# Kernel tuning notes

Hardware: AMD Instinct MI355X
Metric: run time of the kernel (lower is better)

The kernel has to match this reference:

```python
import jax, jax.numpy as jnp
import numpy as np
import math

E, DK, R = 8, 32, 16        # n_experts, d_k, lora rank
SCALING = 16.0 / 16.0        # lora_alpha / r


def setup_inputs() -> dict:
    key = jax.random.key(0)
    ks = jax.random.split(key, 7)
    Bt, S, Din, Dout = 4, 2048, 4096, 4096
    x = jax.random.normal(ks[0], (Bt, S, Din), jnp.float32)
    W = jax.random.normal(ks[1], (Dout, Din), jnp.float32) * 0.02   # base linear weight
    b = jnp.zeros((Dout,), jnp.float32)
    Wq = jax.random.normal(ks[2], (E * DK, Din), jnp.float32) * 0.02  # query_layer
    Wk = jax.random.normal(ks[3], (E * DK, Din), jnp.float32) * 0.02  # key_layer
    A = jax.random.normal(ks[4], (E, R, Din), jnp.float32) * 0.02     # lora_As stacked
    Bm = jax.random.normal(ks[5], (E, Dout, R), jnp.float32) * 0.02   # lora_Bs stacked (nonzero for testing)
    return {"x": x, "W": W, "b": b, "Wq": Wq, "Wk": Wk, "A": A, "Bm": Bm}


def reference(x, W, b, Wq, Wk, A, Bm):
    Bt, S, Din = x.shape
    # base linear: y = x @ W.T + b
    result = jnp.einsum('bsi,oi->bso', x, W) + b
    # per-expert attention routing scores
    q = jnp.einsum('bsi,ni->bsn', x, Wq).reshape(Bt, S, E, DK)
    k = jnp.einsum('bsi,ni->bsn', x, Wk).reshape(Bt, S, E, DK)
    scores = jnp.einsum('bsed,bsed->bse', q, k) / math.sqrt(DK)
    w = jax.nn.softmax(scores, axis=-1)                      # [b,s,E]
    # per-expert low-rank projection: [b,s,E,r]
    h = jnp.einsum('bsi,eri->bser', x, A)
    # fused weighted combine through lora_B: avoids [b,s,E,out] intermediate
    combined = jnp.einsum('bse,bser,eor->bso', w, h, Bm) * SCALING
    return result + combined
```

## Files before the change

### kernel.cpp

```cpp
#include <hip/hip_runtime.h>
#include <hip/hip_bf16.h>
#include <cstdint>
#include <cstddef>


#define T_TOK   8192
#define DIN     4096
#define DOUT    4096
#define KEXT    4224
#define NQKA    640
#define SCALING 1.0f

typedef __attribute__((ext_vector_type(8))) short bf16x8;
typedef __attribute__((ext_vector_type(4))) float f32x4;

__device__ __forceinline__ unsigned short f2bf(float f) {
    __hip_bfloat16 h = __float2bfloat16(f);
    return *reinterpret_cast<unsigned short*>(&h);
}

__device__ __forceinline__ void load_lds16(const void* g, void* l) {
    __builtin_amdgcn_global_load_lds((__attribute__((address_space(1))) void*)g,
                                     (__attribute__((address_space(3))) void*)l,
                                     16, 0, 0);
}

__global__ __launch_bounds__(256) void conv_x(const float4* __restrict__ x,
                                              unsigned short* __restrict__ Aext) {
    int t = blockIdx.x * 256 + threadIdx.x;
    int row = t >> 10, c4 = t & 1023;
    float4 v = x[(size_t)row * 1024 + c4];
    ushort4 o;
    o.x = f2bf(v.x); o.y = f2bf(v.y); o.z = f2bf(v.z); o.w = f2bf(v.w);
    *(ushort4*)&Aext[(size_t)row * KEXT + c4 * 4] = o;
}

__global__ __launch_bounds__(256) void conv_w(const float4* __restrict__ W,
                                              unsigned short* __restrict__ Wext) {
    int t = blockIdx.x * 256 + threadIdx.x;
    int row = t >> 10, c4 = t & 1023;
    float4 v = W[(size_t)row * 1024 + c4];
    ushort4 o;
    o.x = f2bf(v.x); o.y = f2bf(v.y); o.z = f2bf(v.z); o.w = f2bf(v.w);
    *(ushort4*)&Wext[(size_t)row * KEXT + c4 * 4] = o;
}

__global__ __launch_bounds__(256) void fill_bm(const float* __restrict__ Bm,
                                               unsigned short* __restrict__ Wext) {
    int t = blockIdx.x * 256 + threadIdx.x;
    int o = t >> 7, j = t & 127;
    int e = j >> 4, r = j & 15;
    float v = Bm[(size_t)e * (DOUT * 16) + (size_t)o * 16 + r] * SCALING;
    Wext[(size_t)o * KEXT + DIN + j] = f2bf(v);
}

__global__ __launch_bounds__(256) void conv_wqka(const float4* __restrict__ Wq,
                                                 const float4* __restrict__ Wk,
                                                 const float4* __restrict__ Alora,
                                                 unsigned short* __restrict__ Wqka) {
    int t = blockIdx.x * 256 + threadIdx.x;
    int row = t >> 10, c4 = t & 1023;
    float4 v;
    if (row < 256)       v = Wq[(size_t)row * 1024 + c4];
    else if (row < 512)  v = Wk[(size_t)(row - 256) * 1024 + c4];
    else                 v = Alora[(size_t)(row - 512) * 1024 + c4];
    ushort4 o;
    o.x = f2bf(v.x); o.y = f2bf(v.y); o.z = f2bf(v.z); o.w = f2bf(v.w);
    *(ushort4*)&Wqka[(size_t)row * 4096 + c4 * 4] = o;
}

__global__ __launch_bounds__(64) void routing(const float* __restrict__ P,
                                              unsigned short* __restrict__ Aext) {
    int token = blockIdx.x;
    const float* p = P + (size_t)token * NQKA;
    int l = threadIdx.x;
    int e = l >> 3, s = l & 7;
    float pp = 0.f;
#pragma unroll
    for (int j = 0; j < 4; j++) {
        int d = e * 32 + s * 4 + j;
        pp += p[d] * p[256 + d];
    }
    pp += __shfl_xor(pp, 4);
    pp += __shfl_xor(pp, 2);
    pp += __shfl_xor(pp, 1);
    float score = pp * 0.17677669529663687f;
    float mx = score;
    mx = fmaxf(mx, __shfl_xor(mx, 8));
    mx = fmaxf(mx, __shfl_xor(mx, 16));
    mx = fmaxf(mx, __shfl_xor(mx, 32));
    float ex = expf(score - mx);
    float sm = ex;
    sm += __shfl_xor(sm, 8);
    sm += __shfl_xor(sm, 16);
    sm += __shfl_xor(sm, 32);
    float w = ex / sm;
    __shared__ float sw[8];
    if (s == 0) sw[e] = w;
    __syncthreads();
    unsigned short* g = Aext + (size_t)token * KEXT + DIN;
#pragma unroll
    for (int i = 0; i < 2; i++) {
        int j = l + i * 64;
        float val = sw[j >> 4] * p[512 + j] * SCALING;
        g[j] = f2bf(val);
    }
}

__global__ __launch_bounds__(256, 2)
void gemm_bt(const unsigned short* __restrict__ A,
             const unsigned short* __restrict__ B,
             float* __restrict__ C,
             const float* __restrict__ bias,
             int lda, int ldb, int N, int K) {
    __shared__ unsigned short ldsA[128 * 32];
    __shared__ unsigned short ldsB[128 * 32];
    const int t = threadIdx.x;
    const int m0 = blockIdx.y * 128;
    const int n0 = blockIdx.x * 128;
    const int wave = t >> 6, lane = t & 63;
    const int wm = (wave >> 1) * 64, wn = (wave & 1) * 64;
    const int fr = lane & 15, quad = lane >> 4;

    f32x4 acc[4][4];
#pragma unroll
    for (int i = 0; i < 4; i++)
#pragma unroll
        for (int j = 0; j < 4; j++) acc[i][j] = (f32x4){0.f, 0.f, 0.f, 0.f};

    const unsigned short* aptr = A + (size_t)(m0 + (t >> 2)) * lda + (t & 3) * 8;
    const unsigned short* bptr = B + (size_t)(n0 + (t >> 2)) * ldb + (t & 3) * 8;
    char* ldsAb = (char*)ldsA + t * 16;
    char* ldsBb = (char*)ldsB + t * 16;

    for (int k0 = 0; k0 < K; k0 += 32) {
        load_lds16(aptr, ldsAb);
        load_lds16(aptr + 64 * (size_t)lda, ldsAb + 4096);
        load_lds16(bptr, ldsBb);
        load_lds16(bptr + 64 * (size_t)ldb, ldsBb + 4096);
        aptr += 32; bptr += 32;
        __syncthreads();

        bf16x8 af[4], bfr[4];
#pragma unroll
        for (int i = 0; i < 4; i++)
            af[i] = *(const bf16x8*)(ldsA + (wm + i * 16 + fr) * 32 + quad * 8);
#pragma unroll
        for (int j = 0; j < 4; j++)
            bfr[j] = *(const bf16x8*)(ldsB + (wn + j * 16 + fr) * 32 + quad * 8);
#pragma unroll
        for (int i = 0; i < 4; i++)
#pragma unroll
            for (int j = 0; j < 4; j++)
                acc[i][j] = __builtin_amdgcn_mfma_f32_16x16x32_bf16(af[i], bfr[j], acc[i][j], 0, 0, 0);
        __syncthreads();
    }

#pragma unroll
    for (int j = 0; j < 4; j++) {
        int col = n0 + wn + j * 16 + fr;
        float bv = bias ? bias[col] : 0.f;
#pragma unroll
        for (int i = 0; i < 4; i++) {
            int row0 = m0 + wm + i * 16 + quad * 4;
#pragma unroll
            for (int r = 0; r < 4; r++)
                C[(size_t)(row0 + r) * N + col] = acc[i][j][r] + bv;
        }
    }
}

__global__ __launch_bounds__(512, 2)
void gemm256_8p(const unsigned short* __restrict__ A,
                const unsigned short* __restrict__ B,
                float* __restrict__ C,
                const float* __restrict__ bias,
                int lda, int ldb, int N, int K, int grid_n) {
    __shared__ unsigned short lds[65536];
    const int t = threadIdx.x;

    const int nwg = gridDim.x;
    const int q8 = nwg >> 3;
    const int wg = (blockIdx.x & 7) * q8 + (blockIdx.x >> 3);
    const int m0 = (wg / grid_n) * 256;
    const int n0 = (wg % grid_n) * 256;

    const int lane = t & 63;
    const int fr = lane & 15, quad = lane >> 4;
    const int wr = t >> 8;
    const int wc = (t >> 6) & 3;
    const int slot16 = ((quad ^ ((fr >> 1) & 3)) << 4);

    char* ldsA = (char*)lds;
    char* ldsB = (char*)lds + 65536;

    const int srow = t >> 2;
    const int sE = ((t & 3) ^ ((t >> 3) & 3)) * 8;
    const unsigned short* aP = A + (size_t)(m0 + srow) * lda + sE;
    const unsigned short* bP = B + (size_t)(n0 + srow) * ldb + sE;
    const size_t a128 = 128 * (size_t)lda, b128 = 128 * (size_t)ldb;
    char* dA = ldsA + t * 16;
    char* dB = ldsB + t * 16;

#define STAGE_A(cc) { const unsigned short* g_ = aP + (size_t)(cc) * 32;          \
        char* d_ = dA + ((cc) & 3) * 16384;                                       \
        load_lds16(g_, d_); load_lds16(g_ + a128, d_ + 8192); }
#define STAGE_B(cc) { const unsigned short* g_ = bP + (size_t)(cc) * 32;          \
        char* d_ = dB + ((cc) & 3) * 16384;                                       \
        load_lds16(g_, d_); load_lds16(g_ + b128, d_ + 8192); }

    f32x4 acc[8][4];
#pragma unroll
    for (int i = 0; i < 8; i++)
#pragma unroll
        for (int j = 0; j < 4; j++) acc[i][j] = (f32x4){0.f, 0.f, 0.f, 0.f};

    STAGE_A(0); STAGE_B(0);
    STAGE_A(1); STAGE_B(1);
    STAGE_A(2); STAGE_B(2);
    asm volatile("s_waitcnt vmcnt(8)" ::: "memory");
    __builtin_amdgcn_s_barrier();

    const int NC = K >> 5;
    const char* rA = ldsA + wr * 8192 + fr * 64 + slot16;
    const char* rB = ldsB + wc * 4096 + fr * 64 + slot16;

    for (int c = 0; c < NC; ++c) {
        const char* cA = rA + (c & 3) * 16384;
        const char* cB = rB + (c & 3) * 16384;
        bf16x8 am[4], bn[4];

#pragma unroll
        for (int i = 0; i < 4; ++i) am[i] = *(const bf16x8*)(cA + i * 1024);
#pragma unroll
        for (int i = 0; i < 4; ++i) bn[i] = *(const bf16x8*)(cB + i * 1024);
        if (c + 3 < NC) STAGE_A(c + 3);
        __builtin_amdgcn_sched_barrier(0);
        __builtin_amdgcn_s_barrier();
        asm volatile("s_waitcnt lgkmcnt(0)" ::: "memory");
        __builtin_amdgcn_sched_barrier(0);
        __builtin_amdgcn_s_setprio(1);
#pragma unroll
        for (int mf = 0; mf < 4; ++mf)
#pragma unroll
            for (int nf = 0; nf < 4; ++nf)
                acc[mf][nf] = __builtin_amdgcn_mfma_f32_16x16x32_bf16(am[mf], bn[nf], acc[mf][nf], 0, 0, 0);
        __builtin_amdgcn_s_setprio(0);
        __builtin_amdgcn_sched_barrier(0);
        __builtin_amdgcn_s_barrier();

#pragma unroll
        for (int i = 0; i < 4; ++i) am[i] = *(const bf16x8*)(cA + (4 + i) * 1024);
        if (c + 3 < NC) STAGE_B(c + 3);
        __builtin_amdgcn_sched_barrier(0);
        __builtin_amdgcn_s_barrier();
        asm volatile("s_waitcnt lgkmcnt(0)" ::: "memory");
        __builtin_amdgcn_sched_barrier(0);
        __builtin_amdgcn_s_setprio(1);
#pragma unroll
        for (int mf = 0; mf < 4; ++mf)
#pragma unroll
            for (int nf = 0; nf < 4; ++nf)
                acc[4 + mf][nf] = __builtin_amdgcn_mfma_f32_16x16x32_bf16(am[mf], bn[nf], acc[4 + mf][nf], 0, 0, 0);
        __builtin_amdgcn_s_setprio(0);
        if (c < NC - 3)       { asm volatile("s_waitcnt vmcnt(8)" ::: "memory"); }
        else if (c == NC - 3) { asm volatile("s_waitcnt vmcnt(4)" ::: "memory"); }
        else if (c == NC - 2) { asm volatile("s_waitcnt vmcnt(0)" ::: "memory"); }
        __builtin_amdgcn_sched_barrier(0);
        __builtin_amdgcn_s_barrier();
    }

#pragma unroll
    for (int nf = 0; nf < 4; ++nf) {
        int col = n0 + wc * 64 + nf * 16 + fr;
        float bv = bias ? bias[col] : 0.f;
#pragma unroll
        for (int mf = 0; mf < 8; ++mf) {
            int row0 = m0 + wr * 128 + mf * 16 + quad * 4;
#pragma unroll
            for (int r = 0; r < 4; ++r)
                C[(size_t)(row0 + r) * N + col] = acc[mf][nf][r] + bv;
        }
    }
#undef STAGE_A
#undef STAGE_B
}

extern "C" void kernel_launch(void* const* d_in, const int* in_sizes, int n_in,
                              void* d_out, int out_size, void* d_ws, size_t ws_size,
                              hipStream_t stream) {
    const float* x  = (const float*)d_in[0];
    const float* W  = (const float*)d_in[1];
    const float* b  = (const float*)d_in[2];
    const float* Wq = (const float*)d_in[3];
    const float* Wk = (const float*)d_in[4];
    const float* Al = (const float*)d_in[5];
    const float* Bm = (const float*)d_in[6];
    float* out = (float*)d_out;

    char* ws = (char*)d_ws;
    unsigned short* Aext = (unsigned short*)ws;
    unsigned short* Wext = (unsigned short*)(ws + 69206016);
    unsigned short* Wqka = (unsigned short*)(ws + 69206016 + 34603008);
    float*          P    = (float*)(ws + 69206016 + 34603008 + 5242880);

    conv_x   <<<T_TOK * 1024 / 256, 256, 0, stream>>>((const float4*)x, Aext);
    conv_w   <<<DOUT * 1024 / 256, 256, 0, stream>>>((const float4*)W, Wext);
    fill_bm  <<<DOUT * 128 / 256, 256, 0, stream>>>(Bm, Wext);
    conv_wqka<<<NQKA * 1024 / 256, 256, 0, stream>>>((const float4*)Wq, (const float4*)Wk,
                                                     (const float4*)Al, Wqka);

    {
        dim3 grid(NQKA / 128, T_TOK / 128);
        gemm_bt<<<grid, 256, 0, stream>>>(Aext, Wqka, P, nullptr, KEXT, 4096, NQKA, 4096);
    }

    routing<<<T_TOK, 64, 0, stream>>>(P, Aext);

    {
        int grid_n = DOUT / 256;
        int nwg = (T_TOK / 256) * grid_n;
        gemm256_8p<<<nwg, 512, 0, stream>>>(Aext, Wext, out, b, KEXT, KEXT, DOUT, KEXT, grid_n);
    }
}
```

Baseline: 640.5 us.

## Switch main GEMM to 32x32x16 MFMA with single-phase K loop

The main 256x256 GEMM replaces 16x16x32 bf16 MFMAs with 32x32x16 MFMAs, so each wave holds 4x2 32x32 accumulator tiles instead of 8x4 16x16 tiles. The two half-step phases per K chunk, each with its own barriers, are merged into one phase that reads all A and B fragments and issues both global-to-LDS stages together. This cuts LDS fragment reads and barrier count per chunk. It raises the number of live fragment registers and changes the LDS swizzle read pattern, which could cause bank conflicts or register pressure.

```diff
diff --git a/kernel.cpp b/kernel.cpp
--- a/kernel.cpp
+++ b/kernel.cpp
@@ -13,6 +13,7 @@
 
 typedef __attribute__((ext_vector_type(8))) short bf16x8;
 typedef __attribute__((ext_vector_type(4))) float f32x4;
+typedef __attribute__((ext_vector_type(16))) float f32x16;
 
 __device__ __forceinline__ unsigned short f2bf(float f) {
     __hip_bfloat16 h = __float2bfloat16(f);
@@ -171,7 +172,7 @@
 }
 
 __global__ __launch_bounds__(512, 2)
-void gemm256_8p(const unsigned short* __restrict__ A,
+void gemm256_32(const unsigned short* __restrict__ A,
                 const unsigned short* __restrict__ B,
                 float* __restrict__ C,
                 const float* __restrict__ bias,
@@ -186,10 +187,12 @@
     const int n0 = (wg % grid_n) * 256;
 
     const int lane = t & 63;
-    const int fr = lane & 15, quad = lane >> 4;
+    const int lrow = lane & 31, h = lane >> 5;
     const int wr = t >> 8;
     const int wc = (t >> 6) & 3;
-    const int slot16 = ((quad ^ ((fr >> 1) & 3)) << 4);
+    const int sw = (lrow >> 1) & 3;
+    const int off0 = (h ^ sw) << 4;
+    const int off1 = off0 ^ 32;
 
     char* ldsA = (char*)lds;
     char* ldsB = (char*)lds + 65536;
@@ -209,11 +212,13 @@
         char* d_ = dB + ((cc) & 3) * 16384;                                       \
         load_lds16(g_, d_); load_lds16(g_ + b128, d_ + 8192); }
 
-    f32x4 acc[8][4];
-#pragma unroll
-    for (int i = 0; i < 8; i++)
-#pragma unroll
-        for (int j = 0; j < 4; j++) acc[i][j] = (f32x4){0.f, 0.f, 0.f, 0.f};
+    f32x16 acc[4][2];
+#pragma unroll
+    for (int i = 0; i < 4; i++)
+#pragma unroll
+        for (int j = 0; j < 2; j++)
+#pragma unroll
+            for (int r = 0; r < 16; r++) acc[i][j][r] = 0.f;
 
     STAGE_A(0); STAGE_B(0);
     STAGE_A(1); STAGE_B(1);
@@ -222,46 +227,36 @@
     __builtin_amdgcn_s_barrier();
 
     const int NC = K >> 5;
-    const char* rA = ldsA + wr * 8192 + fr * 64 + slot16;
-    const char* rB = ldsB + wc * 4096 + fr * 64 + slot16;
+    const char* rA = ldsA + wr * 8192 + lrow * 64;
+    const char* rB = ldsB + wc * 4096 + lrow * 64;
 
     for (int c = 0; c < NC; ++c) {
         const char* cA = rA + (c & 3) * 16384;
         const char* cB = rB + (c & 3) * 16384;
-        bf16x8 am[4], bn[4];
-
-#pragma unroll
-        for (int i = 0; i < 4; ++i) am[i] = *(const bf16x8*)(cA + i * 1024);
-#pragma unroll
-        for (int i = 0; i < 4; ++i) bn[i] = *(const bf16x8*)(cB + i * 1024);
-        if (c + 3 < NC) STAGE_A(c + 3);
+        bf16x8 av[4][2], bv[2][2];
+#pragma unroll
+        for (int mt = 0; mt < 4; ++mt) {
+            av[mt][0] = *(const bf16x8*)(cA + mt * 2048 + off0);
+            av[mt][1] = *(const bf16x8*)(cA + mt * 2048 + off1);
+        }
+#pragma unroll
+        for (int nt = 0; nt < 2; ++nt) {
+            bv[nt][0] = *(const bf16x8*)(cB + nt * 2048 + off0);
+            bv[nt][1] = *(const bf16x8*)(cB + nt * 2048 + off1);
+        }
+        if (c + 3 < NC) { STAGE_A(c + 3); STAGE_B(c + 3); }
         __builtin_amdgcn_sched_barrier(0);
         __builtin_amdgcn_s_barrier();
         asm volatile("s_waitcnt lgkmcnt(0)" ::: "memory");
         __builtin_amdgcn_sched_barrier(0);
         __builtin_amdgcn_s_setprio(1);
 #pragma unroll
-        for (int mf = 0; mf < 4; ++mf)
-#pragma unroll
-            for (int nf = 0; nf < 4; ++nf)
-                acc[mf][nf] = __builtin_amdgcn_mfma_f32_16x16x32_bf16(am[mf], bn[nf], acc[mf][nf], 0, 0, 0);
-        __builtin_amdgcn_s_setprio(0);
-        __builtin_amdgcn_sched_barrier(0);
-        __builtin_amdgcn_s_barrier();
-
-#pragma unroll
-        for (int i = 0; i < 4; ++i) am[i] = *(const bf16x8*)(cA + (4 + i) * 1024);
-        if (c + 3 < NC) STAGE_B(c + 3);
-        __builtin_amdgcn_sched_barrier(0);
-        __builtin_amdgcn_s_barrier();
-        asm volatile("s_waitcnt lgkmcnt(0)" ::: "memory");
-        __builtin_amdgcn_sched_barrier(0);
-        __builtin_amdgcn_s_setprio(1);
-#pragma unroll
-        for (int mf = 0; mf < 4; ++mf)
-#pragma unroll
-            for (int nf = 0; nf < 4; ++nf)
-                acc[4 + mf][nf] = __builtin_amdgcn_mfma_f32_16x16x32_bf16(am[mf], bn[nf], acc[4 + mf][nf], 0, 0, 0);
+        for (int k = 0; k < 2; ++k)
+#pragma unroll
+            for (int mt = 0; mt < 4; ++mt)
+#pragma unroll
+                for (int nt = 0; nt < 2; ++nt)
+                    acc[mt][nt] = __builtin_amdgcn_mfma_f32_32x32x16_bf16(av[mt][k], bv[nt][k], acc[mt][nt], 0, 0, 0);
         __builtin_amdgcn_s_setprio(0);
         if (c < NC - 3)       { asm volatile("s_waitcnt vmcnt(8)" ::: "memory"); }
         else if (c == NC - 3) { asm volatile("s_waitcnt vmcnt(4)" ::: "memory"); }
@@ -271,15 +266,17 @@
     }
 
 #pragma unroll
-    for (int nf = 0; nf < 4; ++nf) {
-        int col = n0 + wc * 64 + nf * 16 + fr;
-        float bv = bias ? bias[col] : 0.f;
-#pragma unroll
-        for (int mf = 0; mf < 8; ++mf) {
-            int row0 = m0 + wr * 128 + mf * 16 + quad * 4;
-#pragma unroll
-            for (int r = 0; r < 4; ++r)
-                C[(size_t)(row0 + r) * N + col] = acc[mf][nf][r] + bv;
+    for (int nt = 0; nt < 2; ++nt) {
+        int col = n0 + wc * 64 + nt * 32 + lrow;
+        float bvv = bias ? bias[col] : 0.f;
+#pragma unroll
+        for (int mt = 0; mt < 4; ++mt) {
+            int rowb = m0 + wr * 128 + mt * 32 + 4 * h;
+#pragma unroll
+            for (int r = 0; r < 16; ++r) {
+                int row = rowb + (r & 3) + 8 * (r >> 2);
+                C[(size_t)row * N + col] = acc[mt][nt][r] + bvv;
+            }
         }
     }
 #undef STAGE_A
@@ -320,6 +317,6 @@
     {
         int grid_n = DOUT / 256;
         int nwg = (T_TOK / 256) * grid_n;
-        gemm256_8p<<<nwg, 512, 0, stream>>>(Aext, Wext, out, b, KEXT, KEXT, DOUT, KEXT, grid_n);
-    }
-}
+        gemm256_32<<<nwg, 512, 0, stream>>>(Aext, Wext, out, b, KEXT, KEXT, DOUT, KEXT, grid_n);
+    }
+}
```

New measurement: 659.8 us. 3.0% more time.
